# Performance work log

Measured on AMD Instinct MI355X. Metric: run time of the kernel, lower is better.

Reference implementation:

```python
import jax, jax.numpy as jnp
import numpy as np

B, L, D, H = 2, 2048, 512, 8
HD = D // H  # head_dim used only for the concat/reshape trick


def setup_inputs() -> dict:
    key = jax.random.key(0)
    ks = jax.random.split(key, 7)
    s = 0.02  # small init so softmax isn't saturated
    return {
        "q": jax.random.normal(ks[0], (B, L, D), jnp.float32),
        "k": jax.random.normal(ks[1], (B, L, D), jnp.float32),
        "v": jax.random.normal(ks[2], (B, L, D), jnp.float32),
        # per-head full-width projections: W[h] is the nn.Linear weight [out,in]
        "Wq": jax.random.normal(ks[3], (H, D, D), jnp.float32) * s,
        "Wk": jax.random.normal(ks[4], (H, D, D), jnp.float32) * s,
        "Wv": jax.random.normal(ks[5], (H, D, D), jnp.float32) * s,
        # output_layer Linear(d_model*num_heads -> d_model, bias=False)
        "Wo": jax.random.normal(ks[6], (D, H * D), jnp.float32) * s,
    }


def reference(q, k, v, Wq, Wk, Wv, Wo):
    # Each head applies its own full d_model x d_model projections (Linear: x @ W^T)
    qh = jnp.einsum('bld,hed->bhle', q, Wq)  # [B,H,L,D]
    kh = jnp.einsum('bld,hed->bhle', k, Wk)
    vh = jnp.einsum('bld,hed->bhle', v, Wv)
    # scaled by sqrt(d_k) with d_k = d_model (as in the original code)
    scores = jnp.einsum('bhle,bhme->bhlm', qh, kh) / jnp.sqrt(jnp.float32(D))
    attn = jax.nn.softmax(scores, axis=-1)          # [B,H,L,L] (dropout = identity in eval)
    ctx = jnp.einsum('bhlm,bhme->bhle', attn, vh)   # [B,H,L,D]
    # torch: each head ctx [B,L,D] -> view(B,L,H,HD); cat over heads on last dim -> [B,L,H,H*HD]; flatten
    comb = ctx.reshape(B, H, L, H, HD).transpose(0, 2, 3, 1, 4).reshape(B, L, H * D)
    out = comb @ Wo.T                               # [B,L,D]
    return out, attn
```

## Files before the change

### kernel.cpp

```cpp
#include <hip/hip_runtime.h>
#include <cstdio>
#include <cstdint>


#define AS1 __attribute__((address_space(1)))
#define AS3 __attribute__((address_space(3)))

typedef __attribute__((ext_vector_type(8))) short bf16x8;
typedef __attribute__((ext_vector_type(4))) short short4v;
typedef __attribute__((ext_vector_type(4))) float f32x4;

constexpr int cB = 2, cH = 8, cL = 2048, cD = 512;
constexpr float SCORE_SCALE = 0.044194173824159216f;

__device__ __forceinline__ short f2bf(float f) {
  return __builtin_bit_cast(short, static_cast<__bf16>(f));
}

__device__ __forceinline__ void gload16(const void* g, void* l) {
  __builtin_amdgcn_global_load_lds((AS1 const void*)g, (AS3 void*)l, 16, 0, 0);
}

struct CvtArgs { const float4* s[7]; short4v* d[7]; };

__global__ __launch_bounds__(256) void cvt_all(CvtArgs a) {
  const int z = blockIdx.y;
  const int i = blockIdx.x * 256 + threadIdx.x;
  const float4 v = a.s[z][i];
  short4v o = { f2bf(v.x), f2bf(v.y), f2bf(v.z), f2bf(v.w) };
  a.d[z][i] = o;
}

enum { M_PROJ = 0, M_PROJV = 1, M_SCORES = 2, M_OUT = 3 };

template <int MODE>
__global__ __launch_bounds__(256) void gemm_nt(const short* __restrict__ Ap,
                                               const short* __restrict__ Bp,
                                               void* __restrict__ Cp) {
  constexpr int K   = (MODE == M_OUT) ? 2048 : 512;
  constexpr int LDA = (MODE == M_OUT) ? 4096 : 512;
  constexpr int LDB = (MODE == M_OUT) ? 4096 : 512;

  __shared__ short As[128 * 32];
  __shared__ short Bs[128 * 32];

  const int t = threadIdx.x;
  const int lane = t & 63;
  const int wv = t >> 6;
  const int wm = wv >> 1, wn = wv & 1;
  const int z = blockIdx.z;

  size_t Aoff, Boff;
  if constexpr (MODE == M_PROJ || MODE == M_PROJV) {
    Aoff = (size_t)(z >> 3) * ((size_t)cL * cD);
    Boff = (size_t)(z & 7) * ((size_t)cD * cD);
  } else if constexpr (MODE == M_SCORES) {
    Aoff = (size_t)z * ((size_t)cL * cD);
    Boff = (size_t)z * ((size_t)cL * cD);
  } else {
    Aoff = (size_t)(z >> 1) * ((size_t)cL * 4096) + (size_t)(z & 1) * 2048;
    Boff = (size_t)(z & 1) * 2048;
  }

  const short* Ag0 = Ap + Aoff + (size_t)(blockIdx.y * 128) * LDA;
  const short* Bg0 = Bp + Boff + (size_t)(blockIdx.x * 128) * LDB;

  f32x4 acc[4][4];
#pragma unroll
  for (int i = 0; i < 4; ++i)
#pragma unroll
    for (int j = 0; j < 4; ++j) acc[i][j] = (f32x4){0.f, 0.f, 0.f, 0.f};

  for (int kt = 0; kt < K; kt += 32) {
    __syncthreads();
#pragma unroll
    for (int r = 0; r < 2; ++r) {
      const int cbase = r * 256 + wv * 64;
      const int c = cbase + lane;
      const int row = c >> 2, col = (c & 3) * 8;
      gload16(Ag0 + (size_t)row * LDA + kt + col, &As[cbase * 8]);
    }
#pragma unroll
    for (int r = 0; r < 2; ++r) {
      const int cbase = r * 256 + wv * 64;
      const int c = cbase + lane;
      const int row = c >> 2, col = (c & 3) * 8;
      gload16(Bg0 + (size_t)row * LDB + kt + col, &Bs[cbase * 8]);
    }
    __syncthreads();

    const int koff = (lane >> 4) * 8;
    const int ar = wm * 64 + (lane & 15);
    const int br = wn * 64 + (lane & 15);
    bf16x8 af[4], bfv[4];
#pragma unroll
    for (int i = 0; i < 4; ++i) af[i] = *(const bf16x8*)&As[(ar + i * 16) * 32 + koff];
#pragma unroll
    for (int j = 0; j < 4; ++j) bfv[j] = *(const bf16x8*)&Bs[(br + j * 16) * 32 + koff];
#pragma unroll
    for (int i = 0; i < 4; ++i)
#pragma unroll
      for (int j = 0; j < 4; ++j)
        acc[i][j] = __builtin_amdgcn_mfma_f32_16x16x32_bf16(af[i], bfv[j], acc[i][j], 0, 0, 0);
  }

  const int r0 = (lane >> 4) * 4;
  const int cc = lane & 15;
  const int rowbase = blockIdx.y * 128 + wm * 64 + r0;
  const int colbase = blockIdx.x * 128 + wn * 64 + cc;

  if constexpr (MODE == M_PROJ) {
    short* C = (short*)Cp + (size_t)z * ((size_t)cL * cD);
#pragma unroll
    for (int i = 0; i < 4; ++i)
#pragma unroll
      for (int j = 0; j < 4; ++j)
#pragma unroll
        for (int r = 0; r < 4; ++r)
          C[(size_t)(rowbase + i * 16 + r) * cD + (colbase + j * 16)] = f2bf(acc[i][j][r]);
  } else if constexpr (MODE == M_PROJV) {
    short* C = (short*)Cp + (size_t)z * ((size_t)cD * cL);
#pragma unroll
    for (int i = 0; i < 4; ++i)
#pragma unroll
      for (int j = 0; j < 4; ++j) {
        short4v o = { f2bf(acc[i][j][0]), f2bf(acc[i][j][1]),
                      f2bf(acc[i][j][2]), f2bf(acc[i][j][3]) };
        *(short4v*)&C[(size_t)(colbase + j * 16) * cL + (rowbase + i * 16)] = o;
      }
  } else if constexpr (MODE == M_SCORES) {
    float* C = (float*)Cp + (size_t)z * ((size_t)cL * cL);
#pragma unroll
    for (int i = 0; i < 4; ++i)
#pragma unroll
      for (int j = 0; j < 4; ++j)
#pragma unroll
        for (int r = 0; r < 4; ++r)
          C[(size_t)(rowbase + i * 16 + r) * cL + (colbase + j * 16)] =
              acc[i][j][r] * SCORE_SCALE;
  } else {
    float* C = (float*)Cp + (size_t)((z & 1) * 2 + (z >> 1)) * ((size_t)cL * cD);
#pragma unroll
    for (int i = 0; i < 4; ++i)
#pragma unroll
      for (int j = 0; j < 4; ++j)
#pragma unroll
        for (int r = 0; r < 4; ++r)
          C[(size_t)(rowbase + i * 16 + r) * cD + (colbase + j * 16)] = acc[i][j][r];
  }
}

__global__ __launch_bounds__(256) void row_stats(const float* __restrict__ attn,
                                                 float2* __restrict__ stats) {
  const int row = blockIdx.x * 4 + (threadIdx.x >> 6);
  const int lane = threadIdx.x & 63;
  const float4* p = (const float4*)(attn + (size_t)row * cL);
  float4 v[8];
#pragma unroll
  for (int r = 0; r < 8; ++r) v[r] = p[lane + 64 * r];
  float m = -1e30f;
#pragma unroll
  for (int r = 0; r < 8; ++r)
    m = fmaxf(m, fmaxf(fmaxf(v[r].x, v[r].y), fmaxf(v[r].z, v[r].w)));
#pragma unroll
  for (int off = 32; off; off >>= 1) m = fmaxf(m, __shfl_xor(m, off, 64));
  float s = 0.f;
#pragma unroll
  for (int r = 0; r < 8; ++r)
    s += __expf(v[r].x - m) + __expf(v[r].y - m) +
         __expf(v[r].z - m) + __expf(v[r].w - m);
#pragma unroll
  for (int off = 32; off; off >>= 1) s += __shfl_xor(s, off, 64);
  if (lane == 0) stats[row] = make_float2(m, 1.0f / s);
}

__global__ __launch_bounds__(512) void fused_ctx(const short* __restrict__ vhT,
                                                 const float2* __restrict__ stats,
                                                 float* __restrict__ attn,
                                                 short* __restrict__ comb) {
  __shared__ short Pb[128 * 32];
  __shared__ short Bs[512 * 32];

  const int t = threadIdx.x;
  const int lane = t & 63;
  const int wv = t >> 6;
  const int wm = wv >> 2, wn = wv & 3;
  const int rowblk = blockIdx.x;
  const int z = blockIdx.y;

  const int trow = t >> 2;
  const int tcb = t & 3;
  const int tslot = tcb ^ (trow & 3);
  const int grow = rowblk * 128 + trow;
  float* sp = attn + ((size_t)z * cL + grow) * cL + tcb * 8;
  const float2 st = stats[(size_t)z * cL + grow];
  const float m = st.x, invl = st.y;

  const short* Bg = vhT + (size_t)z * ((size_t)cD * cL);

  f32x4 acc[4][8];
#pragma unroll
  for (int i = 0; i < 4; ++i)
#pragma unroll
    for (int j = 0; j < 8; ++j) acc[i][j] = (f32x4){0.f, 0.f, 0.f, 0.f};

  const int sw = ((lane >> 4) ^ (lane & 3)) * 8;
  const int ar = wm * 64 + (lane & 15);
  const int br = wn * 128 + (lane & 15);

  float4 c0 = *(const float4*)(sp);
  float4 c1 = *(const float4*)(sp + 4);

  for (int kt = 0; kt < cL; kt += 32) {
    __syncthreads();
#pragma unroll
    for (int r = 0; r < 4; ++r) {
      const int cbase = r * 512 + wv * 64;
      const int c = cbase + lane;
      const int row = c >> 2;
      const int swcol = ((c & 3) ^ (row & 3)) * 8;
      gload16(Bg + (size_t)row * cL + kt + swcol, &Bs[cbase * 8]);
    }
    {
      const float p0 = __expf(c0.x - m) * invl;
      const float p1 = __expf(c0.y - m) * invl;
      const float p2 = __expf(c0.z - m) * invl;
      const float p3 = __expf(c0.w - m) * invl;
      const float p4 = __expf(c1.x - m) * invl;
      const float p5 = __expf(c1.y - m) * invl;
      const float p6 = __expf(c1.z - m) * invl;
      const float p7 = __expf(c1.w - m) * invl;
      *(float4*)(sp + kt)     = make_float4(p0, p1, p2, p3);
      *(float4*)(sp + kt + 4) = make_float4(p4, p5, p6, p7);
      bf16x8 pb = { f2bf(p0), f2bf(p1), f2bf(p2), f2bf(p3),
                    f2bf(p4), f2bf(p5), f2bf(p6), f2bf(p7) };
      *(bf16x8*)&Pb[trow * 32 + tslot * 8] = pb;
      if (kt + 32 < cL) {
        c0 = *(const float4*)(sp + kt + 32);
        c1 = *(const float4*)(sp + kt + 36);
      }
    }
    __syncthreads();

    bf16x8 af[4], bfv[8];
#pragma unroll
    for (int i = 0; i < 4; ++i) af[i] = *(const bf16x8*)&Pb[(ar + i * 16) * 32 + sw];
#pragma unroll
    for (int j = 0; j < 8; ++j) bfv[j] = *(const bf16x8*)&Bs[(br + j * 16) * 32 + sw];
#pragma unroll
    for (int i = 0; i < 4; ++i)
#pragma unroll
      for (int j = 0; j < 8; ++j)
        acc[i][j] = __builtin_amdgcn_mfma_f32_16x16x32_bf16(af[i], bfv[j], acc[i][j], 0, 0, 0);
  }

  const int r0 = (lane >> 4) * 4;
  const int cc = lane & 15;
  short* C = comb + (size_t)(z >> 3) * ((size_t)cL * (cH * cD));
  const int h = z & 7;
  const int rowbase = rowblk * 128 + wm * 64 + r0;
#pragma unroll
  for (int i = 0; i < 4; ++i)
#pragma unroll
    for (int j = 0; j < 8; ++j) {
      const int e = wn * 128 + j * 16 + cc;
      const int jc = ((e >> 6) << 9) + (h << 6) + (e & 63);
#pragma unroll
      for (int r = 0; r < 4; ++r)
        C[(size_t)(rowbase + i * 16 + r) * (cH * cD) + jc] = f2bf(acc[i][j][r]);
    }
}

__global__ __launch_bounds__(256) void add_halves(const float4* __restrict__ p,
                                                  float4* __restrict__ out) {
  const int i = blockIdx.x * 256 + threadIdx.x;
  const float4 a = p[i];
  const float4 b = p[i + (cB * cL * cD) / 4];
  out[i] = make_float4(a.x + b.x, a.y + b.y, a.z + b.z, a.w + b.w);
}

extern "C" void kernel_launch(void* const* d_in, const int* in_sizes, int n_in,
                              void* d_out, int out_size, void* d_ws, size_t ws_size,
                              hipStream_t stream) {
  (void)in_sizes; (void)n_in; (void)out_size;

  const float* q  = (const float*)d_in[0];
  const float* k  = (const float*)d_in[1];
  const float* v  = (const float*)d_in[2];
  const float* Wq = (const float*)d_in[3];
  const float* Wk = (const float*)d_in[4];
  const float* Wv = (const float*)d_in[5];
  const float* Wo = (const float*)d_in[6];

  float* out  = (float*)d_out;
  float* attn = out + (size_t)cB * cL * cD;

  constexpr size_t Mi = 1ull << 20;
  char* ws = (char*)d_ws;
  short* qbf = (short*)(ws + 0 * Mi);
  short* kbf = (short*)(ws + 4 * Mi);
  short* vbf = (short*)(ws + 8 * Mi);
  short* wqb = (short*)(ws + 12 * Mi);
  short* wkb = (short*)(ws + 16 * Mi);
  short* wvb = (short*)(ws + 20 * Mi);
  short* wob = (short*)(ws + 24 * Mi);
  short* qh  = (short*)(ws + 28 * Mi);
  short* kh  = (short*)(ws + 60 * Mi);
  short* vhT = (short*)(ws + 92 * Mi);
  short* comb = qh;
  float2* stats = (float2*)(ws + 0 * Mi);
  float*  pout  = (float*)(ws + 60 * Mi);

  if (ws_size < 124 * Mi) {
    fprintf(stderr, "kernel_launch: ws too small (%zu < %zu)\n", ws_size, 124 * Mi);
    return;
  }

  CvtArgs ca;
  ca.s[0] = (const float4*)q;  ca.d[0] = (short4v*)qbf;
  ca.s[1] = (const float4*)k;  ca.d[1] = (short4v*)kbf;
  ca.s[2] = (const float4*)v;  ca.d[2] = (short4v*)vbf;
  ca.s[3] = (const float4*)Wq; ca.d[3] = (short4v*)wqb;
  ca.s[4] = (const float4*)Wk; ca.d[4] = (short4v*)wkb;
  ca.s[5] = (const float4*)Wv; ca.d[5] = (short4v*)wvb;
  ca.s[6] = (const float4*)Wo; ca.d[6] = (short4v*)wob;
  cvt_all<<<dim3(2048, 7), 256, 0, stream>>>(ca);

  gemm_nt<M_PROJ ><<<dim3(4, 16, 16), 256, 0, stream>>>(qbf, wqb, qh);
  gemm_nt<M_PROJ ><<<dim3(4, 16, 16), 256, 0, stream>>>(kbf, wkb, kh);
  gemm_nt<M_PROJV><<<dim3(4, 16, 16), 256, 0, stream>>>(vbf, wvb, vhT);

  gemm_nt<M_SCORES><<<dim3(16, 16, 16), 256, 0, stream>>>(qh, kh, attn);

  row_stats<<<cB * cH * cL / 4, 256, 0, stream>>>(attn, stats);

  fused_ctx<<<dim3(16, cB * cH), 512, 0, stream>>>(vhT, stats, attn, comb);

  gemm_nt<M_OUT><<<dim3(4, 16, 4), 256, 0, stream>>>(comb, wob, (void*)pout);

  add_halves<<<2048, 256, 0, stream>>>((const float4*)pout, (float4*)out);
}
```

Measured before the change: 828.6 us.

## Fuse partial softmax stats into scores GEMM and double-buffer fused_ctx

The scores GEMM epilogue now computes per-row partial max and sum-of-exp over each 64-column slice and writes them to a partial-stats buffer. A small combine kernel merges these partials, replacing the row_stats pass that re-read the full fp32 attention matrix. The fused_ctx kernel is also restructured with double-buffered LDS for P and V tiles, a changed swizzle, manual waitcnt/barrier scheduling and raised priority around the MFMAs, so loads overlap compute. This adds epilogue shuffle work to the scores GEMM and relies on careful hand-placed synchronisation.

Measured after the change: 773.0 us. 6.7% less time.

```diff
diff --git a/kernel.cpp b/kernel.cpp
--- a/kernel.cpp
+++ b/kernel.cpp
@@ -36,7 +36,8 @@
 template <int MODE>
 __global__ __launch_bounds__(256) void gemm_nt(const short* __restrict__ Ap,
                                                const short* __restrict__ Bp,
-                                               void* __restrict__ Cp) {
+                                               void* __restrict__ Cp,
+                                               float2* __restrict__ Sp) {
   constexpr int K   = (MODE == M_OUT) ? 2048 : 512;
   constexpr int LDA = (MODE == M_OUT) ? 4096 : 512;
   constexpr int LDB = (MODE == M_OUT) ? 4096 : 512;
@@ -130,14 +131,33 @@
       }
   } else if constexpr (MODE == M_SCORES) {
     float* C = (float*)Cp + (size_t)z * ((size_t)cL * cL);
-#pragma unroll
-    for (int i = 0; i < 4; ++i)
+    float2* ps = Sp + (size_t)z * ((size_t)cL * 32);
+    const int pid = blockIdx.x * 2 + wn;
+#pragma unroll
+    for (int i = 0; i < 4; ++i) {
+      float sv[4][4];
+#pragma unroll
+      for (int j = 0; j < 4; ++j)
+#pragma unroll
+        for (int r = 0; r < 4; ++r) sv[j][r] = acc[i][j][r] * SCORE_SCALE;
 #pragma unroll
       for (int j = 0; j < 4; ++j)
 #pragma unroll
         for (int r = 0; r < 4; ++r)
-          C[(size_t)(rowbase + i * 16 + r) * cL + (colbase + j * 16)] =
-              acc[i][j][r] * SCORE_SCALE;
+          C[(size_t)(rowbase + i * 16 + r) * cL + (colbase + j * 16)] = sv[j][r];
+#pragma unroll
+      for (int r = 0; r < 4; ++r) {
+        float mx = fmaxf(fmaxf(sv[0][r], sv[1][r]), fmaxf(sv[2][r], sv[3][r]));
+#pragma unroll
+        for (int off = 1; off < 16; off <<= 1) mx = fmaxf(mx, __shfl_xor(mx, off, 64));
+        float sm = __expf(sv[0][r] - mx) + __expf(sv[1][r] - mx) +
+                   __expf(sv[2][r] - mx) + __expf(sv[3][r] - mx);
+#pragma unroll
+        for (int off = 1; off < 16; off <<= 1) sm += __shfl_xor(sm, off, 64);
+        if ((lane & 15) == 0)
+          ps[(size_t)(rowbase + i * 16 + r) * 32 + pid] = make_float2(mx, sm);
+      }
+    }
   } else {
     float* C = (float*)Cp + (size_t)((z & 1) * 2 + (z >> 1)) * ((size_t)cL * cD);
 #pragma unroll
@@ -150,36 +170,25 @@
   }
 }
 
-__global__ __launch_bounds__(256) void row_stats(const float* __restrict__ attn,
-                                                 float2* __restrict__ stats) {
-  const int row = blockIdx.x * 4 + (threadIdx.x >> 6);
-  const int lane = threadIdx.x & 63;
-  const float4* p = (const float4*)(attn + (size_t)row * cL);
-  float4 v[8];
-#pragma unroll
-  for (int r = 0; r < 8; ++r) v[r] = p[lane + 64 * r];
+__global__ __launch_bounds__(256) void combine_stats(const float2* __restrict__ ps,
+                                                     float2* __restrict__ stats) {
+  const int row = blockIdx.x * 256 + threadIdx.x;
+  const float2* p = ps + (size_t)row * 32;
   float m = -1e30f;
 #pragma unroll
-  for (int r = 0; r < 8; ++r)
-    m = fmaxf(m, fmaxf(fmaxf(v[r].x, v[r].y), fmaxf(v[r].z, v[r].w)));
-#pragma unroll
-  for (int off = 32; off; off >>= 1) m = fmaxf(m, __shfl_xor(m, off, 64));
-  float s = 0.f;
-#pragma unroll
-  for (int r = 0; r < 8; ++r)
-    s += __expf(v[r].x - m) + __expf(v[r].y - m) +
-         __expf(v[r].z - m) + __expf(v[r].w - m);
-#pragma unroll
-  for (int off = 32; off; off >>= 1) s += __shfl_xor(s, off, 64);
-  if (lane == 0) stats[row] = make_float2(m, 1.0f / s);
+  for (int i = 0; i < 32; ++i) m = fmaxf(m, p[i].x);
+  float l = 0.f;
+#pragma unroll
+  for (int i = 0; i < 32; ++i) l += p[i].y * __expf(p[i].x - m);
+  stats[row] = make_float2(m, 1.0f / l);
 }
 
 __global__ __launch_bounds__(512) void fused_ctx(const short* __restrict__ vhT,
                                                  const float2* __restrict__ stats,
                                                  float* __restrict__ attn,
                                                  short* __restrict__ comb) {
-  __shared__ short Pb[128 * 32];
-  __shared__ short Bs[512 * 32];
+  __shared__ short Bs[2][512 * 32];
+  __shared__ short Pb[2][128 * 32];
 
   const int t = threadIdx.x;
   const int lane = t & 63;
@@ -190,7 +199,7 @@
 
   const int trow = t >> 2;
   const int tcb = t & 3;
-  const int tslot = tcb ^ (trow & 3);
+  const int tslot = tcb ^ ((trow >> 1) & 3);
   const int grow = rowblk * 128 + trow;
   float* sp = attn + ((size_t)z * cL + grow) * cL + tcb * 8;
   const float2 st = stats[(size_t)z * cL + grow];
@@ -204,54 +213,101 @@
 #pragma unroll
     for (int j = 0; j < 8; ++j) acc[i][j] = (f32x4){0.f, 0.f, 0.f, 0.f};
 
-  const int sw = ((lane >> 4) ^ (lane & 3)) * 8;
+  const int qk = lane >> 4;
   const int ar = wm * 64 + (lane & 15);
   const int br = wn * 128 + (lane & 15);
 
-  float4 c0 = *(const float4*)(sp);
-  float4 c1 = *(const float4*)(sp + 4);
-
-  for (int kt = 0; kt < cL; kt += 32) {
-    __syncthreads();
+  auto stageB = [&](int nb, int kt) {
 #pragma unroll
     for (int r = 0; r < 4; ++r) {
       const int cbase = r * 512 + wv * 64;
       const int c = cbase + lane;
       const int row = c >> 2;
-      const int swcol = ((c & 3) ^ (row & 3)) * 8;
-      gload16(Bg + (size_t)row * cL + kt + swcol, &Bs[cbase * 8]);
-    }
-    {
-      const float p0 = __expf(c0.x - m) * invl;
-      const float p1 = __expf(c0.y - m) * invl;
-      const float p2 = __expf(c0.z - m) * invl;
-      const float p3 = __expf(c0.w - m) * invl;
-      const float p4 = __expf(c1.x - m) * invl;
-      const float p5 = __expf(c1.y - m) * invl;
-      const float p6 = __expf(c1.z - m) * invl;
-      const float p7 = __expf(c1.w - m) * invl;
-      *(float4*)(sp + kt)     = make_float4(p0, p1, p2, p3);
-      *(float4*)(sp + kt + 4) = make_float4(p4, p5, p6, p7);
-      bf16x8 pb = { f2bf(p0), f2bf(p1), f2bf(p2), f2bf(p3),
-                    f2bf(p4), f2bf(p5), f2bf(p6), f2bf(p7) };
-      *(bf16x8*)&Pb[trow * 32 + tslot * 8] = pb;
-      if (kt + 32 < cL) {
-        c0 = *(const float4*)(sp + kt + 32);
-        c1 = *(const float4*)(sp + kt + 36);
-      }
-    }
-    __syncthreads();
-
+      const int swcol = ((c & 3) ^ ((row >> 1) & 3)) * 8;
+      gload16(Bg + (size_t)row * cL + kt + swcol, &Bs[nb][cbase * 8]);
+    }
+  };
+  auto transform = [&](int ck, float4 v0, float4 v1) -> bf16x8 {
+    float* dst = sp + ck * 32;
+    const float p0 = __expf(v0.x - m) * invl;
+    const float p1 = __expf(v0.y - m) * invl;
+    const float p2 = __expf(v0.z - m) * invl;
+    const float p3 = __expf(v0.w - m) * invl;
+    const float p4 = __expf(v1.x - m) * invl;
+    const float p5 = __expf(v1.y - m) * invl;
+    const float p6 = __expf(v1.z - m) * invl;
+    const float p7 = __expf(v1.w - m) * invl;
+    *(float4*)(dst)     = make_float4(p0, p1, p2, p3);
+    *(float4*)(dst + 4) = make_float4(p4, p5, p6, p7);
+    bf16x8 pb = { f2bf(p0), f2bf(p1), f2bf(p2), f2bf(p3),
+                  f2bf(p4), f2bf(p5), f2bf(p6), f2bf(p7) };
+    return pb;
+  };
+
+  stageB(0, 0);
+  float4 c0 = *(const float4*)(sp);
+  float4 c1 = *(const float4*)(sp + 4);
+  bf16x8 pb = transform(0, c0, c1);
+  c0 = *(const float4*)(sp + 32);
+  c1 = *(const float4*)(sp + 36);
+  *(bf16x8*)&Pb[0][trow * 32 + tslot * 8] = pb;
+
+  for (int k = 0; k < 63; ++k) {
+    const int cb = k & 1, nb = cb ^ 1;
+    pb = transform(k + 1, c0, c1);
+    const int kc = (k + 2) & 63;
+    c0 = *(const float4*)(sp + kc * 32);
+    c1 = *(const float4*)(sp + kc * 32 + 4);
+    asm volatile("s_waitcnt vmcnt(4) lgkmcnt(0)" ::: "memory");
+    __builtin_amdgcn_sched_barrier(0);
+    __builtin_amdgcn_s_barrier();
+    __builtin_amdgcn_sched_barrier(0);
+    *(bf16x8*)&Pb[nb][trow * 32 + tslot * 8] = pb;
+    stageB(nb, (k + 1) * 32);
+    __builtin_amdgcn_sched_barrier(0);
     bf16x8 af[4], bfv[8];
 #pragma unroll
-    for (int i = 0; i < 4; ++i) af[i] = *(const bf16x8*)&Pb[(ar + i * 16) * 32 + sw];
-#pragma unroll
-    for (int j = 0; j < 8; ++j) bfv[j] = *(const bf16x8*)&Bs[(br + j * 16) * 32 + sw];
+    for (int i = 0; i < 4; ++i) {
+      const int rA = ar + i * 16;
+      af[i] = *(const bf16x8*)&Pb[cb][rA * 32 + (qk ^ ((rA >> 1) & 3)) * 8];
+    }
+#pragma unroll
+    for (int j = 0; j < 8; ++j) {
+      const int rB = br + j * 16;
+      bfv[j] = *(const bf16x8*)&Bs[cb][rB * 32 + (qk ^ ((rB >> 1) & 3)) * 8];
+    }
+    __builtin_amdgcn_s_setprio(1);
 #pragma unroll
     for (int i = 0; i < 4; ++i)
 #pragma unroll
       for (int j = 0; j < 8; ++j)
         acc[i][j] = __builtin_amdgcn_mfma_f32_16x16x32_bf16(af[i], bfv[j], acc[i][j], 0, 0, 0);
+    __builtin_amdgcn_s_setprio(0);
+  }
+
+  asm volatile("s_waitcnt vmcnt(0) lgkmcnt(0)" ::: "memory");
+  __builtin_amdgcn_sched_barrier(0);
+  __builtin_amdgcn_s_barrier();
+  __builtin_amdgcn_sched_barrier(0);
+  {
+    bf16x8 af[4], bfv[8];
+#pragma unroll
+    for (int i = 0; i < 4; ++i) {
+      const int rA = ar + i * 16;
+      af[i] = *(const bf16x8*)&Pb[1][rA * 32 + (qk ^ ((rA >> 1) & 3)) * 8];
+    }
+#pragma unroll
+    for (int j = 0; j < 8; ++j) {
+      const int rB = br + j * 16;
+      bfv[j] = *(const bf16x8*)&Bs[1][rB * 32 + (qk ^ ((rB >> 1) & 3)) * 8];
+    }
+    __builtin_amdgcn_s_setprio(1);
+#pragma unroll
+    for (int i = 0; i < 4; ++i)
+#pragma unroll
+      for (int j = 0; j < 8; ++j)
+        acc[i][j] = __builtin_amdgcn_mfma_f32_16x16x32_bf16(af[i], bfv[j], acc[i][j], 0, 0, 0);
+    __builtin_amdgcn_s_setprio(0);
   }
 
   const int r0 = (lane >> 4) * 4;
@@ -308,8 +364,9 @@
   short* kh  = (short*)(ws + 60 * Mi);
   short* vhT = (short*)(ws + 92 * Mi);
   short* comb = qh;
-  float2* stats = (float2*)(ws + 0 * Mi);
-  float*  pout  = (float*)(ws + 60 * Mi);
+  float2* stats  = (float2*)(ws + 0 * Mi);
+  float2* pstats = (float2*)(ws + 4 * Mi);
+  float*  pout   = (float*)(ws + 60 * Mi);
 
   if (ws_size < 124 * Mi) {
     fprintf(stderr, "kernel_launch: ws too small (%zu < %zu)\n", ws_size, 124 * Mi);
@@ -326,17 +383,17 @@
   ca.s[6] = (const float4*)Wo; ca.d[6] = (short4v*)wob;
   cvt_all<<<dim3(2048, 7), 256, 0, stream>>>(ca);
 
-  gemm_nt<M_PROJ ><<<dim3(4, 16, 16), 256, 0, stream>>>(qbf, wqb, qh);
-  gemm_nt<M_PROJ ><<<dim3(4, 16, 16), 256, 0, stream>>>(kbf, wkb, kh);
-  gemm_nt<M_PROJV><<<dim3(4, 16, 16), 256, 0, stream>>>(vbf, wvb, vhT);
-
-  gemm_nt<M_SCORES><<<dim3(16, 16, 16), 256, 0, stream>>>(qh, kh, attn);
-
-  row_stats<<<cB * cH * cL / 4, 256, 0, stream>>>(attn, stats);
+  gemm_nt<M_PROJ ><<<dim3(4, 16, 16), 256, 0, stream>>>(qbf, wqb, qh, nullptr);
+  gemm_nt<M_PROJ ><<<dim3(4, 16, 16), 256, 0, stream>>>(kbf, wkb, kh, nullptr);
+  gemm_nt<M_PROJV><<<dim3(4, 16, 16), 256, 0, stream>>>(vbf, wvb, vhT, nullptr);
+
+  gemm_nt<M_SCORES><<<dim3(16, 16, 16), 256, 0, stream>>>(qh, kh, attn, pstats);
+
+  combine_stats<<<cB * cH * cL / 256, 256, 0, stream>>>(pstats, stats);
 
   fused_ctx<<<dim3(16, cB * cH), 512, 0, stream>>>(vhT, stats, attn, comb);
 
-  gemm_nt<M_OUT><<<dim3(4, 16, 4), 256, 0, stream>>>(comb, wob, (void*)pout);
+  gemm_nt<M_OUT><<<dim3(4, 16, 4), 256, 0, stream>>>(comb, wob, (void*)pout, nullptr);
 
   add_halves<<<2048, 256, 0, stream>>>((const float4*)pout, (float4*)out);
 }
```
